# Performance work log

Measured on AMD Instinct MI355X. Metric: run time of the kernel, lower is better.

The kernel has to match this reference:

```python
import jax, jax.numpy as jnp
import numpy as np

H = 64  # hidden_size
IN = 1  # input_size
OUT = 7  # output_size
B, T = 4096, 512


def setup_inputs() -> dict:
    key = jax.random.key(0)
    ks = jax.random.split(key, 11)
    s = 1.0 / np.sqrt(H)  # PyTorch LSTM init scale
    u = lambda k, shp: jax.random.uniform(k, shp, jnp.float32, -s, s)
    return {
        "x": jax.random.normal(ks[0], (B, T, IN), jnp.float32),
        # layer 0
        "Wih0": u(ks[1], (4 * H, IN)),
        "Whh0": u(ks[2], (4 * H, H)),
        "bih0": u(ks[3], (4 * H,)),
        "bhh0": u(ks[4], (4 * H,)),
        # layer 1
        "Wih1": u(ks[5], (4 * H, H)),
        "Whh1": u(ks[6], (4 * H, H)),
        "bih1": u(ks[7], (4 * H,)),
        "bhh1": u(ks[8], (4 * H,)),
        # fc head
        "Wfc": u(ks[9], (OUT, H)),
        "bfc": u(ks[10], (OUT,)),
    }


def _lstm_layer(x, Wih, Whh, bih, bhh):
    """x: [B, T, F] -> hidden sequence [B, T, H]. PyTorch gate order i,f,g,o."""
    b, t, _ = x.shape
    h = Whh.shape[1]
    # precompute input contribution for all timesteps: [T, B, 4H]
    xg = (jnp.einsum('btf,gf->btg', x, Wih) + bih + bhh).transpose(1, 0, 2)
    WhhT = Whh.T  # [H, 4H]

    def step(carry, g_t):
        h_t, c_t = carry
        gates = g_t + h_t @ WhhT  # [B, 4H]
        i, f, g, o = jnp.split(gates, 4, axis=-1)
        i = jax.nn.sigmoid(i)
        f = jax.nn.sigmoid(f)
        g = jnp.tanh(g)
        o = jax.nn.sigmoid(o)
        c_new = f * c_t + i * g
        h_new = o * jnp.tanh(c_new)
        return (h_new, c_new), h_new

    h0 = jnp.zeros((b, h), x.dtype)
    c0 = jnp.zeros((b, h), x.dtype)
    (_, _), hs = jax.lax.scan(step, (h0, c0), xg)
    return hs.transpose(1, 0, 2)  # [B, T, H]


def reference(x, Wih0, Whh0, bih0, bhh0, Wih1, Whh1, bih1, bhh1, Wfc, bfc):
    h1 = _lstm_layer(x, Wih0, Whh0, bih0, bhh0)   # dropout between layers is identity in eval
    h2 = _lstm_layer(h1, Wih1, Whh1, bih1, bhh1)
    last = h2[:, -1, :]  # [B, H]; dropout identity in eval
    return last @ Wfc.T + bfc  # [B, OUT]
```

## Files before the change

### kernel.cpp

```cpp
#include <hip/hip_runtime.h>
#include <hip/hip_bf16.h>

#define HH 64
#define TT 512
#define BB 16

typedef __attribute__((ext_vector_type(8))) short short8;
typedef __attribute__((ext_vector_type(4))) float f32x4;

static __device__ __forceinline__ unsigned short f2bf(float f) {
  unsigned u = __float_as_uint(f);
  u += 0x7fffu + ((u >> 16) & 1u);
  return (unsigned short)(u >> 16);
}

static __device__ __forceinline__ float sigm(float x) {
  float e = __builtin_amdgcn_exp2f(-1.442695041f * x);
  return __builtin_amdgcn_rcpf(1.0f + e);
}
static __device__ __forceinline__ float tanh_fast(float x) {
  float e = __builtin_amdgcn_exp2f(2.885390082f * x);
  return 1.0f - 2.0f * __builtin_amdgcn_rcpf(1.0f + e);
}

static __device__ __forceinline__ short8 pack8(const float* __restrict__ p) {
  const float4* p4 = (const float4*)p;
  float4 a = p4[0], b = p4[1];
  short8 r;
  r[0] = (short)f2bf(a.x); r[1] = (short)f2bf(a.y);
  r[2] = (short)f2bf(a.z); r[3] = (short)f2bf(a.w);
  r[4] = (short)f2bf(b.x); r[5] = (short)f2bf(b.y);
  r[6] = (short)f2bf(b.z); r[7] = (short)f2bf(b.w);
  return r;
}

#define MF(A, B, C) __builtin_amdgcn_mfma_f32_16x16x32_bf16((A), (B), (C), 0, 0, 0)

#define STEP_A(P, XP) {                                                        \
    const char* rd = (const char*)h0buf[(P) ^ 1];                              \
    short8 af0 = *(const short8*)(rd + rdo0);                                  \
    short8 af1 = *(const short8*)(rd + rdo1);                                  \
    f32x4 xv = *(const f32x4*)(XP);                                            \
    f32x4 a0 = MF(af0, wf[0], bs[0]); a0 = MF(af1, wf[1], a0);                 \
    f32x4 a1 = MF(af0, wf[2], bs[1]); a1 = MF(af1, wf[3], a1);                 \
    f32x4 a2 = MF(af0, wf[4], bs[2]); a2 = MF(af1, wf[5], a2);                 \
    f32x4 a3 = MF(af0, wf[6], bs[3]); a3 = MF(af1, wf[7], a3);                 \
    char* wrb = (char*)h0buf[P];                                               \
    _Pragma("unroll")                                                          \
    for (int j = 0; j < 4; ++j) {                                              \
      float pi = fmaf(xv[j], wx[0], a0[j]);                                    \
      float pf = fmaf(xv[j], wx[1], a1[j]);                                    \
      float pg = fmaf(xv[j], wx[2], a2[j]);                                    \
      float po = fmaf(xv[j], wx[3], a3[j]);                                    \
      float iv = sigm(pi), fv = sigm(pf);                                      \
      float gv = tanh_fast(pg), ov = sigm(po);                                 \
      float c = fmaf(fv, cst[j], iv * gv);                                     \
      cst[j] = c;                                                              \
      float h = ov * tanh_fast(c);                                             \
      *(__hip_bfloat16*)(wrb + wro[j]) = __float2bfloat16(h);                  \
    }                                                                          \
  }

#define STEP_B(P, LAST) {                                                      \
    const char* rd0 = (const char*)h0buf[(P) ^ 1];                             \
    const char* rd1 = (const char*)h1buf[P];                                   \
    short8 af0 = *(const short8*)(rd0 + rdo0);                                 \
    short8 af1 = *(const short8*)(rd0 + rdo1);                                 \
    short8 af2 = *(const short8*)(rd1 + rdo0);                                 \
    short8 af3 = *(const short8*)(rd1 + rdo1);                                 \
    f32x4 a0 = MF(af0, wf[0],  bs[0]); a0 = MF(af1, wf[1],  a0);               \
    a0 = MF(af2, wf[2],  a0);  a0 = MF(af3, wf[3],  a0);                       \
    f32x4 a1 = MF(af0, wf[4],  bs[1]); a1 = MF(af1, wf[5],  a1);               \
    a1 = MF(af2, wf[6],  a1);  a1 = MF(af3, wf[7],  a1);                       \
    f32x4 a2 = MF(af0, wf[8],  bs[2]); a2 = MF(af1, wf[9],  a2);               \
    a2 = MF(af2, wf[10], a2);  a2 = MF(af3, wf[11], a2);                       \
    f32x4 a3 = MF(af0, wf[12], bs[3]); a3 = MF(af1, wf[13], a3);               \
    a3 = MF(af2, wf[14], a3);  a3 = MF(af3, wf[15], a3);                       \
    char* wrb = (char*)h1buf[(P) ^ 1];                                         \
    _Pragma("unroll")                                                          \
    for (int j = 0; j < 4; ++j) {                                              \
      float iv = sigm(a0[j]), fv = sigm(a1[j]);                                \
      float gv = tanh_fast(a2[j]), ov = sigm(a3[j]);                           \
      float c = fmaf(fv, cst[j], iv * gv);                                     \
      cst[j] = c;                                                              \
      float h = ov * tanh_fast(c);                                             \
      *(__hip_bfloat16*)(wrb + wro[j]) = __float2bfloat16(h);                  \
      if (LAST) h1f[(q * 4 + j) * HH + colw] = h;                              \
    }                                                                          \
  }

__global__ __launch_bounds__(512, 2)
void lstm2_fused(const float* __restrict__ x,
                 const float* __restrict__ Wih0, const float* __restrict__ Whh0,
                 const float* __restrict__ bih0, const float* __restrict__ bhh0,
                 const float* __restrict__ Wih1, const float* __restrict__ Whh1,
                 const float* __restrict__ bih1, const float* __restrict__ bhh1,
                 const float* __restrict__ Wfc,  const float* __restrict__ bfc,
                 float* __restrict__ out)
{
  __shared__ float xs[TT * BB];
  __shared__ __align__(16) unsigned short h0buf[2][BB * HH];
  __shared__ __align__(16) unsigned short h1buf[2][BB * HH];
  __shared__ float h1f[BB * HH];

  const int tid  = threadIdx.x;
  const int wave = tid >> 6;
  const int lane = tid & 63;
  const int grp  = wave >> 2;
  const int w    = wave & 3;
  const int m    = lane & 15;
  const int q    = lane >> 4;
  const int b0   = blockIdx.x * BB;

  {
    const int t = tid;
    #pragma unroll
    for (int r = 0; r < BB; ++r)
      xs[t * BB + r] = x[(size_t)(b0 + r) * TT + t];
  }
  ((unsigned int*)h0buf)[tid] = 0; ((unsigned int*)h0buf)[tid + 512] = 0;
  ((unsigned int*)h1buf)[tid] = 0; ((unsigned int*)h1buf)[tid + 512] = 0;

  short8 wf[16];
  f32x4 bs[4];
  float wx[4];
  #pragma unroll
  for (int n = 0; n < 4; ++n) {
    const int colg = 16 * (4 * n + w) + m;
    if (grp == 0) {
      const float b = bih0[colg] + bhh0[colg];
      bs[n][0] = b; bs[n][1] = b; bs[n][2] = b; bs[n][3] = b;
      wx[n] = Wih0[colg];
      #pragma unroll
      for (int kt = 0; kt < 2; ++kt)
        wf[n * 2 + kt] = pack8(Whh0 + colg * HH + kt * 32 + q * 8);
    } else {
      const float b = bih1[colg] + bhh1[colg];
      bs[n][0] = b; bs[n][1] = b; bs[n][2] = b; bs[n][3] = b;
      wx[n] = 0.f;
      #pragma unroll
      for (int kt = 0; kt < 4; ++kt) {
        const float* Wsrc = (kt < 2) ? Wih1 : Whh1;
        wf[n * 4 + kt] = pack8(Wsrc + colg * HH + (kt & 1) * 32 + q * 8);
      }
    }
  }

  const int colw = 16 * w + m;
  const int rdo0 = m * 128 + ((q * 16) ^ ((m & 7) << 4));
  const int rdo1 = m * 128 + ((64 + q * 16) ^ ((m & 7) << 4));
  int wro[4];
  #pragma unroll
  for (int j = 0; j < 4; ++j) {
    const int row = q * 4 + j;
    wro[j] = row * 128 + ((2 * colw) ^ ((row & 7) << 4));
  }

  __syncthreads();

  float cst[4] = {0.f, 0.f, 0.f, 0.f};
  const float* xp = xs + q * 4;

  if (grp == 0) { STEP_A(0, xp) }
  xp += BB;
  __syncthreads();

  #pragma unroll 1
  for (int k = 0; k < (TT - 2) / 2; ++k) {
    if (grp == 0) { STEP_A(1, xp) } else { STEP_B(1, false) }
    xp += BB;
    __syncthreads();
    if (grp == 0) { STEP_A(0, xp) } else { STEP_B(0, false) }
    xp += BB;
    __syncthreads();
  }
  if (grp == 0) { STEP_A(1, xp) } else { STEP_B(1, false) }
  __syncthreads();
  if (grp == 1) { STEP_B(0, true) }
  __syncthreads();

  if (tid < BB * 7) {
    const int b = tid / 7, o = tid % 7;
    float s = bfc[o];
    #pragma unroll
    for (int k = 0; k < HH; ++k) s = fmaf(h1f[b * HH + k], Wfc[o * HH + k], s);
    out[(size_t)(b0 + b) * 7 + o] = s;
  }
}

extern "C" void kernel_launch(void* const* d_in, const int* in_sizes, int n_in,
                              void* d_out, int out_size, void* d_ws, size_t ws_size,
                              hipStream_t stream) {
  const float* x    = (const float*)d_in[0];
  const float* Wih0 = (const float*)d_in[1];
  const float* Whh0 = (const float*)d_in[2];
  const float* bih0 = (const float*)d_in[3];
  const float* bhh0 = (const float*)d_in[4];
  const float* Wih1 = (const float*)d_in[5];
  const float* Whh1 = (const float*)d_in[6];
  const float* bih1 = (const float*)d_in[7];
  const float* bhh1 = (const float*)d_in[8];
  const float* Wfc  = (const float*)d_in[9];
  const float* bfc  = (const float*)d_in[10];
  float* out = (float*)d_out;

  dim3 grid(4096 / BB);
  dim3 block(512);
  hipLaunchKernelGGL(lstm2_fused, grid, block, 0, stream,
                     x, Wih0, Whh0, bih0, bhh0, Wih1, Whh1, bih1, bhh1, Wfc, bfc, out);
}
```

Measured before the change: 371.0 us.

## Replace block barriers with per-wave LDS flag spin-waits and a 4-deep h0 ring

```diff
diff --git a/kernel.cpp b/kernel.cpp
--- a/kernel.cpp
+++ b/kernel.cpp
@@ -36,16 +36,33 @@
 
 #define MF(A, B, C) __builtin_amdgcn_mfma_f32_16x16x32_bf16((A), (B), (C), 0, 0, 0)
 
-#define STEP_A(P, XP) {                                                        \
-    const char* rd = (const char*)h0buf[(P) ^ 1];                              \
+static __device__ __forceinline__ void spin2(volatile int* fa, int ta,
+                                             volatile int* fb, int tb) {
+  for (;;) {
+    int a0 = fa[0], a1 = fa[1], a2 = fa[2], a3 = fa[3];
+    int b0 = fb[0], b1 = fb[1], b2 = fb[2], b3 = fb[3];
+    if (((a0 >= ta) & (a1 >= ta) & (a2 >= ta) & (a3 >= ta) &
+         (b0 >= tb) & (b1 >= tb) & (b2 >= tb) & (b3 >= tb)) != 0)
+      break;
+  }
+  asm volatile("" ::: "memory");
+}
+
+#define PUBLISH(FLAGP, VAL) {                                   \
+    asm volatile("s_waitcnt lgkmcnt(0)" ::: "memory");          \
+    if (lane == 0) *(volatile int*)(FLAGP) = (VAL);             \
+  }
+
+#define STEP_A(RD, WR) {                                                       \
+    const char* rd = (const char*)(RD);                                        \
     short8 af0 = *(const short8*)(rd + rdo0);                                  \
     short8 af1 = *(const short8*)(rd + rdo1);                                  \
-    f32x4 xv = *(const f32x4*)(XP);                                            \
+    f32x4 xv = *(const f32x4*)(xp); xp += BB;                                  \
     f32x4 a0 = MF(af0, wf[0], bs[0]); a0 = MF(af1, wf[1], a0);                 \
     f32x4 a1 = MF(af0, wf[2], bs[1]); a1 = MF(af1, wf[3], a1);                 \
     f32x4 a2 = MF(af0, wf[4], bs[2]); a2 = MF(af1, wf[5], a2);                 \
     f32x4 a3 = MF(af0, wf[6], bs[3]); a3 = MF(af1, wf[7], a3);                 \
-    char* wrb = (char*)h0buf[P];                                               \
+    char* wrb = (char*)(WR);                                                   \
     _Pragma("unroll")                                                          \
     for (int j = 0; j < 4; ++j) {                                              \
       float pi = fmaf(xv[j], wx[0], a0[j]);                                    \
@@ -61,9 +78,9 @@
     }                                                                          \
   }
 
-#define STEP_B(P, LAST) {                                                      \
-    const char* rd0 = (const char*)h0buf[(P) ^ 1];                             \
-    const char* rd1 = (const char*)h1buf[P];                                   \
+#define STEP_B(RD0, RD1, WR, LAST) {                                           \
+    const char* rd0 = (const char*)(RD0);                                      \
+    const char* rd1 = (const char*)(RD1);                                      \
     short8 af0 = *(const short8*)(rd0 + rdo0);                                 \
     short8 af1 = *(const short8*)(rd0 + rdo1);                                 \
     short8 af2 = *(const short8*)(rd1 + rdo0);                                 \
@@ -76,7 +93,7 @@
     a2 = MF(af2, wf[10], a2);  a2 = MF(af3, wf[11], a2);                       \
     f32x4 a3 = MF(af0, wf[12], bs[3]); a3 = MF(af1, wf[13], a3);               \
     a3 = MF(af2, wf[14], a3);  a3 = MF(af3, wf[15], a3);                       \
-    char* wrb = (char*)h1buf[(P) ^ 1];                                         \
+    char* wrb = (char*)(WR);                                                   \
     _Pragma("unroll")                                                          \
     for (int j = 0; j < 4; ++j) {                                              \
       float iv = sigm(a0[j]), fv = sigm(a1[j]);                                \
@@ -99,9 +116,10 @@
                  float* __restrict__ out)
 {
   __shared__ float xs[TT * BB];
-  __shared__ __align__(16) unsigned short h0buf[2][BB * HH];
+  __shared__ __align__(16) unsigned short h0ring[4][BB * HH];
   __shared__ __align__(16) unsigned short h1buf[2][BB * HH];
   __shared__ float h1f[BB * HH];
+  __shared__ int flagA[4], flagB[4];
 
   const int tid  = threadIdx.x;
   const int wave = tid >> 6;
@@ -118,8 +136,10 @@
     for (int r = 0; r < BB; ++r)
       xs[t * BB + r] = x[(size_t)(b0 + r) * TT + t];
   }
-  ((unsigned int*)h0buf)[tid] = 0; ((unsigned int*)h0buf)[tid + 512] = 0;
+  ((unsigned int*)h0ring)[tid]        = 0; ((unsigned int*)h0ring)[tid + 512]  = 0;
+  ((unsigned int*)h0ring)[tid + 1024] = 0; ((unsigned int*)h0ring)[tid + 1536] = 0;
   ((unsigned int*)h1buf)[tid] = 0; ((unsigned int*)h1buf)[tid + 512] = 0;
+  if (tid < 4) { flagA[tid] = 0; flagB[tid] = 0; }
 
   short8 wf[16];
   f32x4 bs[4];
@@ -159,24 +179,37 @@
   __syncthreads();
 
   float cst[4] = {0.f, 0.f, 0.f, 0.f};
-  const float* xp = xs + q * 4;
-
-  if (grp == 0) { STEP_A(0, xp) }
-  xp += BB;
-  __syncthreads();
-
-  #pragma unroll 1
-  for (int k = 0; k < (TT - 2) / 2; ++k) {
-    if (grp == 0) { STEP_A(1, xp) } else { STEP_B(1, false) }
-    xp += BB;
-    __syncthreads();
-    if (grp == 0) { STEP_A(0, xp) } else { STEP_B(0, false) }
-    xp += BB;
-    __syncthreads();
-  }
-  if (grp == 0) { STEP_A(1, xp) } else { STEP_B(1, false) }
-  __syncthreads();
-  if (grp == 1) { STEP_B(0, true) }
+
+  if (grp == 0) {
+    const float* xp = xs + q * 4;
+    #pragma unroll 1
+    for (int k = 0; k < TT / 4; ++k) {
+      const int t0 = 4 * k;
+      spin2(flagA, t0,     flagB, t0 - 3);
+      STEP_A(h0ring[3], h0ring[0])  PUBLISH(&flagA[w], t0 + 1);
+      spin2(flagA, t0 + 1, flagB, t0 - 2);
+      STEP_A(h0ring[0], h0ring[1])  PUBLISH(&flagA[w], t0 + 2);
+      spin2(flagA, t0 + 2, flagB, t0 - 1);
+      STEP_A(h0ring[1], h0ring[2])  PUBLISH(&flagA[w], t0 + 3);
+      spin2(flagA, t0 + 3, flagB, t0);
+      STEP_A(h0ring[2], h0ring[3])  PUBLISH(&flagA[w], t0 + 4);
+    }
+  } else {
+    #pragma unroll 1
+    for (int k = 0; k < TT / 4; ++k) {
+      const int t1 = 4 * k + 1;
+      const bool last = (k == TT / 4 - 1);
+      spin2(flagA, t1,     flagB, t1 - 1);
+      STEP_B(h0ring[0], h1buf[1], h1buf[0], false)  PUBLISH(&flagB[w], t1);
+      spin2(flagA, t1 + 1, flagB, t1);
+      STEP_B(h0ring[1], h1buf[0], h1buf[1], false)  PUBLISH(&flagB[w], t1 + 1);
+      spin2(flagA, t1 + 2, flagB, t1 + 1);
+      STEP_B(h0ring[2], h1buf[1], h1buf[0], false)  PUBLISH(&flagB[w], t1 + 2);
+      spin2(flagA, t1 + 3, flagB, t1 + 2);
+      STEP_B(h0ring[3], h1buf[0], h1buf[1], last)   PUBLISH(&flagB[w], t1 + 3);
+    }
+  }
+
   __syncthreads();
 
   if (tid < BB * 7) {
```

After: 501.6 us. +35.2%, slower.

## Halve batch rows per block so two blocks share each CU

Applied to the files above, without the earlier changes.

```diff
diff --git a/kernel.cpp b/kernel.cpp
--- a/kernel.cpp
+++ b/kernel.cpp
@@ -3,7 +3,7 @@
 
 #define HH 64
 #define TT 512
-#define BB 16
+#define BB 8
 
 typedef __attribute__((ext_vector_type(8))) short short8;
 typedef __attribute__((ext_vector_type(4))) float f32x4;
@@ -36,29 +36,33 @@
 
 #define MF(A, B, C) __builtin_amdgcn_mfma_f32_16x16x32_bf16((A), (B), (C), 0, 0, 0)
 
-#define STEP_A(P, XP) {                                                        \
+#define ACT_STORE(A0, A1, A2, A3, J, XV, HASX, CSTv, WROv, WRB, LASTF) {       \
+    float pi = (A0)[J], pf = (A1)[J], pg = (A2)[J], po = (A3)[J];              \
+    if (HASX) {                                                                \
+      pi = fmaf((XV), wx[0], pi); pf = fmaf((XV), wx[1], pf);                  \
+      pg = fmaf((XV), wx[2], pg); po = fmaf((XV), wx[3], po);                  \
+    }                                                                          \
+    float iv = sigm(pi), fv = sigm(pf);                                        \
+    float gv = tanh_fast(pg), ov = sigm(po);                                   \
+    float c = fmaf(fv, (CSTv), iv * gv);                                       \
+    (CSTv) = c;                                                                \
+    float h = ov * tanh_fast(c);                                               \
+    *(__hip_bfloat16*)((WRB) + (WROv)) = __float2bfloat16(h);                  \
+    if (LASTF) h1f[(2 * q + (J) / 2) * HH + colw] = h;                         \
+  }
+
+#define STEP_A(P) {                                                            \
     const char* rd = (const char*)h0buf[(P) ^ 1];                              \
     short8 af0 = *(const short8*)(rd + rdo0);                                  \
     short8 af1 = *(const short8*)(rd + rdo1);                                  \
-    f32x4 xv = *(const f32x4*)(XP);                                            \
+    float2 xv = *(const float2*)xpf; xpf += BB;                                \
     f32x4 a0 = MF(af0, wf[0], bs[0]); a0 = MF(af1, wf[1], a0);                 \
     f32x4 a1 = MF(af0, wf[2], bs[1]); a1 = MF(af1, wf[3], a1);                 \
     f32x4 a2 = MF(af0, wf[4], bs[2]); a2 = MF(af1, wf[5], a2);                 \
     f32x4 a3 = MF(af0, wf[6], bs[3]); a3 = MF(af1, wf[7], a3);                 \
     char* wrb = (char*)h0buf[P];                                               \
-    _Pragma("unroll")                                                          \
-    for (int j = 0; j < 4; ++j) {                                              \
-      float pi = fmaf(xv[j], wx[0], a0[j]);                                    \
-      float pf = fmaf(xv[j], wx[1], a1[j]);                                    \
-      float pg = fmaf(xv[j], wx[2], a2[j]);                                    \
-      float po = fmaf(xv[j], wx[3], a3[j]);                                    \
-      float iv = sigm(pi), fv = sigm(pf);                                      \
-      float gv = tanh_fast(pg), ov = sigm(po);                                 \
-      float c = fmaf(fv, cst[j], iv * gv);                                     \
-      cst[j] = c;                                                              \
-      float h = ov * tanh_fast(c);                                             \
-      *(__hip_bfloat16*)(wrb + wro[j]) = __float2bfloat16(h);                  \
-    }                                                                          \
+    ACT_STORE(a0, a1, a2, a3, 0, xv.x, true, cst0, wro0, wrb, false)           \
+    ACT_STORE(a0, a1, a2, a3, 2, xv.y, true, cst1, wro1, wrb, false)           \
   }
 
 #define STEP_B(P, LAST) {                                                      \
@@ -77,19 +81,11 @@
     f32x4 a3 = MF(af0, wf[12], bs[3]); a3 = MF(af1, wf[13], a3);               \
     a3 = MF(af2, wf[14], a3);  a3 = MF(af3, wf[15], a3);                       \
     char* wrb = (char*)h1buf[(P) ^ 1];                                         \
-    _Pragma("unroll")                                                          \
-    for (int j = 0; j < 4; ++j) {                                              \
-      float iv = sigm(a0[j]), fv = sigm(a1[j]);                                \
-      float gv = tanh_fast(a2[j]), ov = sigm(a3[j]);                           \
-      float c = fmaf(fv, cst[j], iv * gv);                                     \
-      cst[j] = c;                                                              \
-      float h = ov * tanh_fast(c);                                             \
-      *(__hip_bfloat16*)(wrb + wro[j]) = __float2bfloat16(h);                  \
-      if (LAST) h1f[(q * 4 + j) * HH + colw] = h;                              \
-    }                                                                          \
-  }
-
-__global__ __launch_bounds__(512, 2)
+    ACT_STORE(a0, a1, a2, a3, 0, 0.f, false, cst0, wro0, wrb, LAST)            \
+    ACT_STORE(a0, a1, a2, a3, 2, 0.f, false, cst1, wro1, wrb, LAST)            \
+  }
+
+__global__ __launch_bounds__(512, 4)
 void lstm2_fused(const float* __restrict__ x,
                  const float* __restrict__ Wih0, const float* __restrict__ Whh0,
                  const float* __restrict__ bih0, const float* __restrict__ bhh0,
@@ -99,8 +95,8 @@
                  float* __restrict__ out)
 {
   __shared__ float xs[TT * BB];
-  __shared__ __align__(16) unsigned short h0buf[2][BB * HH];
-  __shared__ __align__(16) unsigned short h1buf[2][BB * HH];
+  __shared__ __align__(16) unsigned short h0buf[2][16 * HH];
+  __shared__ __align__(16) unsigned short h1buf[2][16 * HH];
   __shared__ float h1f[BB * HH];
 
   const int tid  = threadIdx.x;
@@ -149,32 +145,27 @@
   const int colw = 16 * w + m;
   const int rdo0 = m * 128 + ((q * 16) ^ ((m & 7) << 4));
   const int rdo1 = m * 128 + ((64 + q * 16) ^ ((m & 7) << 4));
-  int wro[4];
-  #pragma unroll
-  for (int j = 0; j < 4; ++j) {
-    const int row = q * 4 + j;
-    wro[j] = row * 128 + ((2 * colw) ^ ((row & 7) << 4));
-  }
-
-  __syncthreads();
-
-  float cst[4] = {0.f, 0.f, 0.f, 0.f};
-  const float* xp = xs + q * 4;
-
-  if (grp == 0) { STEP_A(0, xp) }
-  xp += BB;
+  const int r0 = 4 * q;
+  const int r2 = 4 * q + 2;
+  const int wro0 = r0 * 128 + ((2 * colw) ^ ((r0 & 7) << 4));
+  const int wro1 = r2 * 128 + ((2 * colw) ^ ((r2 & 7) << 4));
+
+  __syncthreads();
+
+  float cst0 = 0.f, cst1 = 0.f;
+  const float* xpf = xs + 2 * q;
+
+  if (grp == 0) { STEP_A(0) }
   __syncthreads();
 
   #pragma unroll 1
   for (int k = 0; k < (TT - 2) / 2; ++k) {
-    if (grp == 0) { STEP_A(1, xp) } else { STEP_B(1, false) }
-    xp += BB;
+    if (grp == 0) { STEP_A(1) } else { STEP_B(1, false) }
     __syncthreads();
-    if (grp == 0) { STEP_A(0, xp) } else { STEP_B(0, false) }
-    xp += BB;
+    if (grp == 0) { STEP_A(0) } else { STEP_B(0, false) }
     __syncthreads();
   }
-  if (grp == 0) { STEP_A(1, xp) } else { STEP_B(1, false) }
+  if (grp == 0) { STEP_A(1) } else { STEP_B(1, false) }
   __syncthreads();
   if (grp == 1) { STEP_B(0, true) }
   __syncthreads();
```

Measured after the change: 426.3 us. 1.15x slower.
